# Kernel tuning notes

Hardware: AMD Instinct MI355X
Metric: run time of the kernel (lower is better)

Reference implementation:

```python
import jax, jax.numpy as jnp
import numpy as np

B, T, C, H = 2, 2048, 1024, 16
HD = C // H  # head dim = 64


def setup_inputs() -> dict:
    key = jax.random.key(0)
    k1, k2, k3 = jax.random.split(key, 3)
    scale = 0.02
    x = jax.random.normal(k1, (B, T, C), dtype=jnp.float32)
    w_attn = jax.random.normal(k2, (C, 3 * C), dtype=jnp.float32) * scale
    b_attn = jnp.zeros((3 * C,), dtype=jnp.float32)
    w_proj = jax.random.normal(k3, (C, C), dtype=jnp.float32) * scale
    b_proj = jnp.zeros((C,), dtype=jnp.float32)
    return {"x": x, "w_attn": w_attn, "b_attn": b_attn, "w_proj": w_proj, "b_proj": b_proj}


def reference(x, w_attn, b_attn, w_proj, b_proj):
    b, t, c = x.shape
    qkv = x @ w_attn + b_attn  # [B,T,3C]
    q, k, v = jnp.split(qkv, 3, axis=-1)
    # [B,T,C] -> [B,H,T,HD]
    q = q.reshape(b, t, H, HD).transpose(0, 2, 1, 3)
    k = k.reshape(b, t, H, HD).transpose(0, 2, 1, 3)
    v = v.reshape(b, t, H, HD).transpose(0, 2, 1, 3)
    att = jnp.einsum('bhqd,bhkd->bhqk', q, k) * (1.0 / jnp.sqrt(jnp.float32(HD)))
    causal = jnp.tril(jnp.ones((t, t), dtype=bool))  # [T,T]
    att = jnp.where(causal[None, None, :, :], att, jnp.float32(-jnp.inf))
    att = jax.nn.softmax(att, axis=-1)
    y = jnp.einsum('bhqk,bhkd->bhqd', att, v)
    y = y.transpose(0, 2, 1, 3).reshape(b, t, c)
    return y @ w_proj + b_proj
```

## Files before the change

kernel.cpp:

```cpp
#include <hip/hip_runtime.h>


typedef unsigned short u16;
typedef unsigned short u16x8 __attribute__((ext_vector_type(8)));
typedef __bf16 bf16x8 __attribute__((ext_vector_type(8)));
typedef __bf16 bf16x4 __attribute__((ext_vector_type(4)));
typedef float f32x4 __attribute__((ext_vector_type(4)));

#define MFMA16(a, b, c) __builtin_amdgcn_mfma_f32_16x16x32_bf16(a, b, c, 0, 0, 0)

static __device__ __forceinline__ u16 f2b(float f) {
  union { float f; unsigned int i; } x; x.f = f;
  unsigned int r = x.i + 0x7fffu + ((x.i >> 16) & 1u);
  return (u16)(r >> 16);
}
static __device__ __forceinline__ float b2f(u16 u) {
  union { unsigned int i; float f; } x; x.i = ((unsigned int)u) << 16; return x.f;
}

static __device__ __forceinline__ void gload_lds16(const u16* g, u16* l) {
#if defined(__HIP_DEVICE_COMPILE__)
  __builtin_amdgcn_global_load_lds(
      (const __attribute__((address_space(1))) unsigned int*)g,
      (__attribute__((address_space(3))) unsigned int*)l,
      16, 0, 0);
#else
  (void)g; (void)l;
#endif
}

__global__ __launch_bounds__(256) void cast_f32_bf16(
    const float* __restrict__ in, u16* __restrict__ out) {
  int i = (blockIdx.x * 256 + threadIdx.x) * 8;
  float4 a = *(const float4*)&in[i];
  float4 b = *(const float4*)&in[i + 4];
  u16x8 o;
  o[0] = f2b(a.x); o[1] = f2b(a.y); o[2] = f2b(a.z); o[3] = f2b(a.w);
  o[4] = f2b(b.x); o[5] = f2b(b.y); o[6] = f2b(b.z); o[7] = f2b(b.w);
  *(u16x8*)&out[i] = o;
}

__global__ __launch_bounds__(256) void transpose_f32_bf16(
    const float* __restrict__ in, u16* __restrict__ out, int R, int Cc) {
  __shared__ u16 tile[32][33];
  int bx = blockIdx.x, by = blockIdx.y;
  int tx = threadIdx.x, ty = threadIdx.y;
#pragma unroll
  for (int i = 0; i < 4; i++) {
    int r = by * 32 + ty + i * 8;
    int c = bx * 32 + tx;
    tile[ty + i * 8][tx] = f2b(in[r * Cc + c]);
  }
  __syncthreads();
#pragma unroll
  for (int i = 0; i < 4; i++) {
    int r = bx * 32 + ty + i * 8;
    int c = by * 32 + tx;
    out[r * R + c] = tile[tx][ty + i * 8];
  }
}

__global__ __launch_bounds__(256) void transpose_v(
    const u16* __restrict__ in, u16* __restrict__ out) {
  int bh = blockIdx.y;
  int t = blockIdx.x * 128 + (threadIdx.x & 127);
  int dg = (threadIdx.x >> 7) * 32;
  const u16* src = in + (bh * 2048 + t) * 64;
  u16* dst = out + bh * 64 * 2048 + t;
#pragma unroll
  for (int i = 0; i < 32; i++) {
    int d = dg + i;
    dst[d * 2048] = src[d];
  }
}

template <int MODE>
__global__ __launch_bounds__(256, 2) void gemm_bt(
    const u16* __restrict__ A, const u16* __restrict__ Bt,
    const float* __restrict__ bias, float* __restrict__ out,
    u16* __restrict__ Qb, u16* __restrict__ Kb, u16* __restrict__ Vb,
    int M, int N, int K) {
  __shared__ u16 lA[128 * 32];
  __shared__ u16 lB[128 * 32];

  const int tid = threadIdx.x;
  const int lane = tid & 63;
  const int w = tid >> 6;
  const int wm = (w >> 1) * 64, wn = (w & 1) * 64;
  const int l15 = lane & 15, quad = lane >> 4;
  const int m0 = blockIdx.y * 128, n0 = blockIdx.x * 128;

  const int srow = lane >> 2;
  const int scol = (lane & 3) * 8;

  f32x4 acc[4][4] = {};

  for (int k0 = 0; k0 < K; k0 += 32) {
    __syncthreads();
#pragma unroll
    for (int h = 0; h < 2; h++) {
      int r = h * 64 + w * 16 + srow;
      gload_lds16(&A[(m0 + r) * K + k0 + scol], &lA[h * 2048 + w * 512 + lane * 8]);
      gload_lds16(&Bt[(n0 + r) * K + k0 + scol], &lB[h * 2048 + w * 512 + lane * 8]);
    }
    __syncthreads();

    bf16x8 af[4], bfr[4];
#pragma unroll
    for (int mi = 0; mi < 4; mi++)
      af[mi] = *(const bf16x8*)&lA[(wm + mi * 16 + l15) * 32 + quad * 8];
#pragma unroll
    for (int ni = 0; ni < 4; ni++)
      bfr[ni] = *(const bf16x8*)&lB[(wn + ni * 16 + l15) * 32 + quad * 8];
#pragma unroll
    for (int mi = 0; mi < 4; mi++)
#pragma unroll
      for (int ni = 0; ni < 4; ni++)
        acc[mi][ni] = MFMA16(af[mi], bfr[ni], acc[mi][ni]);
  }

#pragma unroll
  for (int mi = 0; mi < 4; mi++) {
#pragma unroll
    for (int ni = 0; ni < 4; ni++) {
      int n = n0 + wn + ni * 16 + l15;
      float bv = bias[n];
#pragma unroll
      for (int reg = 0; reg < 4; reg++) {
        int m = m0 + wm + mi * 16 + quad * 4 + reg;
        float v = acc[mi][ni][reg] + bv;
        if (MODE == 1) {
          out[m * N + n] = v;
        } else {
          int which = n >> 10;
          if (which == 1) v *= 0.18033688011112042f;
          int hn = n & 1023;
          int hh = hn >> 6, d = hn & 63;
          int b = m >> 11, t = m & 2047;
          u16* dst = (which == 0) ? Qb : ((which == 1) ? Kb : Vb);
          dst[(((b << 4) + hh) * 2048 + t) * 64 + d] = f2b(v);
        }
      }
    }
  }
}

__global__ __launch_bounds__(256, 4) void attn_split(
    const u16* __restrict__ Qg, const u16* __restrict__ Kg,
    const u16* __restrict__ Vt, u16* __restrict__ Yg,
    u16* __restrict__ Opart, float* __restrict__ lpart) {
  __shared__ u16 lk[64 * 72];
  __shared__ u16 lvt[64 * 72];

  const int x = blockIdx.x;
  const int bh = blockIdx.y;
  int qt, s, ns;
  if (x < 8)       { qt = x;                s = 0;            ns = 1; }
  else if (x < 24) { int r = x - 8;  qt = 8  + (r >> 1); s = r & 1; ns = 2; }
  else if (x < 48) { int r = x - 24; qt = 16 + r / 3;    s = r % 3; ns = 3; }
  else             { int r = x - 48; qt = 24 + (r >> 2); s = r & 3; ns = 4; }
  const int kts = s * 8;
  const int kend = (kts + 8 < qt + 1) ? (kts + 8) : (qt + 1);

  const int tid = threadIdx.x;
  const int lane = tid & 63;
  const int w = tid >> 6;
  const int l15 = lane & 15, quad = lane >> 4;
  const int qbase = qt * 64;
  const int base = bh * 2048 * 64;
  const int vbase = bh * 64 * 2048;

  const int sr = tid >> 3;
  const int sc = (tid & 7) * 8;

  const u16* qrow = Qg + base + (qbase + w * 16 + l15) * 64;
  bf16x8 bq0 = *(const bf16x8*)&qrow[quad * 8];
  bf16x8 bq1 = *(const bf16x8*)&qrow[32 + quad * 8];

  u16x8 onesu = {0x3F80, 0x3F80, 0x3F80, 0x3F80, 0x3F80, 0x3F80, 0x3F80, 0x3F80};
  bf16x8 ones = *(const bf16x8*)&onesu;

  const u16* kp = Kg + base;
  const u16* vp = Vt + vbase;

  u16x8 kr[2], vr[2];
  {
    int kvb = kts * 64;
#pragma unroll
    for (int h = 0; h < 2; h++) {
      int r = sr + h * 32;
      kr[h] = *(const u16x8*)&kp[(kvb + r) * 64 + sc];
      vr[h] = *(const u16x8*)&vp[r * 2048 + kvb + sc];
    }
  }

  f32x4 oacc[4] = {};
  f32x4 lacc = {};

  for (int kt = kts; kt < kend; kt++) {
    __syncthreads();
#pragma unroll
    for (int h = 0; h < 2; h++) {
      int r = sr + h * 32;
      *(u16x8*)&lk[r * 72 + sc] = kr[h];
      *(u16x8*)&lvt[r * 72 + sc] = vr[h];
    }
    __syncthreads();
    if (kt + 1 < kend) {
      int kvb = (kt + 1) * 64;
#pragma unroll
      for (int h = 0; h < 2; h++) {
        int r = sr + h * 32;
        kr[h] = *(const u16x8*)&kp[(kvb + r) * 64 + sc];
        vr[h] = *(const u16x8*)&vp[r * 2048 + kvb + sc];
      }
    }

    const bool diag = (kt == qt);
    const int qloc = w * 16 + l15;

#pragma unroll
    for (int u = 0; u < 2; u++) {
      bf16x8 pa;
#pragma unroll
      for (int half = 0; half < 2; half++) {
        int nt = 2 * u + half;
        bf16x8 ak0 = *(const bf16x8*)&lk[(nt * 16 + l15) * 72 + quad * 8];
        bf16x8 ak1 = *(const bf16x8*)&lk[(nt * 16 + l15) * 72 + 32 + quad * 8];
        f32x4 st = {};
        st = MFMA16(ak0, bq0, st);
        st = MFMA16(ak1, bq1, st);
#pragma unroll
        for (int reg = 0; reg < 4; reg++) {
          float sv = st[reg];
          if (diag && (nt * 16 + quad * 4 + reg) > qloc) sv = -1e30f;
          pa[half * 4 + reg] = (__bf16)exp2f(sv);
        }
      }
      lacc = MFMA16(pa, ones, lacc);
#pragma unroll
      for (int dt = 0; dt < 4; dt++) {
        const u16* vrow = &lvt[(dt * 16 + l15) * 72 + u * 32 + quad * 4];
        bf16x4 lo = *(const bf16x4*)&vrow[0];
        bf16x4 hi = *(const bf16x4*)&vrow[16];
        bf16x8 bv;
#pragma unroll
        for (int j = 0; j < 4; j++) { bv[j] = lo[j]; bv[4 + j] = hi[j]; }
        oacc[dt] = MFMA16(pa, bv, oacc[dt]);
      }
    }
  }

  if (ns == 1) {
    const int b = bh >> 4, hh = bh & 15;
    float inv[4];
#pragma unroll
    for (int reg = 0; reg < 4; reg++) inv[reg] = 1.0f / lacc[reg];
#pragma unroll
    for (int dt = 0; dt < 4; dt++)
#pragma unroll
      for (int reg = 0; reg < 4; reg++) {
        int q = qbase + w * 16 + quad * 4 + reg;
        int col = hh * 64 + dt * 16 + l15;
        Yg[(b * 2048 + q) * 1024 + col] = f2b(oacc[dt][reg] * inv[reg]);
      }
  } else {
    const int p = bh * 80 + x;
    u16* op = Opart + p * 4096 + (w * 16) * 64;
#pragma unroll
    for (int dt = 0; dt < 4; dt++)
#pragma unroll
      for (int reg = 0; reg < 4; reg++)
        op[(quad * 4 + reg) * 64 + dt * 16 + l15] = f2b(oacc[dt][reg]);
    if (l15 == 0) {
#pragma unroll
      for (int reg = 0; reg < 4; reg++)
        lpart[p * 64 + w * 16 + quad * 4 + reg] = lacc[reg];
    }
  }
}

__global__ __launch_bounds__(256) void attn_combine(
    const u16* __restrict__ Opart, const float* __restrict__ lpart,
    u16* __restrict__ Yg) {
  const int qt = 8 + blockIdx.x;
  const int bh = blockIdx.y;
  const int tid = threadIdx.x;
  const int row = tid >> 2;
  const int cg = (tid & 3) * 16;
  int xb, ns;
  if (qt < 16)      { xb = 8  + (qt - 8) * 2;  ns = 2; }
  else if (qt < 24) { xb = 24 + (qt - 16) * 3; ns = 3; }
  else              { xb = 48 + (qt - 24) * 4; ns = 4; }

  float acc[16] = {};
  float lsum = 0.f;
  for (int i = 0; i < ns; i++) {
    int p = bh * 80 + xb + i;
    lsum += lpart[p * 64 + row];
    const u16* oprow = Opart + p * 4096 + row * 64 + cg;
    u16x8 a = *(const u16x8*)&oprow[0];
    u16x8 b = *(const u16x8*)&oprow[8];
#pragma unroll
    for (int j = 0; j < 8; j++) { acc[j] += b2f(a[j]); acc[8 + j] += b2f(b[j]); }
  }
  float inv = 1.0f / lsum;
  u16x8 o0, o1;
#pragma unroll
  for (int j = 0; j < 8; j++) { o0[j] = f2b(acc[j] * inv); o1[j] = f2b(acc[8 + j] * inv); }
  const int b = bh >> 4, hh = bh & 15;
  u16* y = Yg + ((long)(b * 2048 + qt * 64 + row)) * 1024 + hh * 64 + cg;
  *(u16x8*)&y[0] = o0;
  *(u16x8*)&y[8] = o1;
}

__global__ __launch_bounds__(256, 4) void attn_kernel(
    const u16* __restrict__ Qg, const u16* __restrict__ Kg,
    const u16* __restrict__ Vt, u16* __restrict__ Yg) {
  __shared__ u16 lk[64 * 72];
  __shared__ u16 lvt[64 * 72];

  const int qt = 31 - blockIdx.x;
  const int bh = blockIdx.y;
  const int tid = threadIdx.x;
  const int lane = tid & 63;
  const int w = tid >> 6;
  const int l15 = lane & 15, quad = lane >> 4;
  const int qbase = qt * 64;
  const int base = bh * 2048 * 64;
  const int vbase = bh * 64 * 2048;
  const int sr = tid >> 3;
  const int sc = (tid & 7) * 8;

  const u16* qrow = Qg + base + (qbase + w * 16 + l15) * 64;
  bf16x8 bq0 = *(const bf16x8*)&qrow[quad * 8];
  bf16x8 bq1 = *(const bf16x8*)&qrow[32 + quad * 8];

  u16x8 onesu = {0x3F80, 0x3F80, 0x3F80, 0x3F80, 0x3F80, 0x3F80, 0x3F80, 0x3F80};
  bf16x8 ones = *(const bf16x8*)&onesu;

  const u16* kp = Kg + base;
  const u16* vp = Vt + vbase;

  u16x8 kr[2], vr[2];
#pragma unroll
  for (int h = 0; h < 2; h++) {
    int r = sr + h * 32;
    kr[h] = *(const u16x8*)&kp[r * 64 + sc];
    vr[h] = *(const u16x8*)&vp[r * 2048 + sc];
  }

  f32x4 oacc[4] = {};
  f32x4 lacc = {};

  for (int kt = 0; kt <= qt; kt++) {
    __syncthreads();
#pragma unroll
    for (int h = 0; h < 2; h++) {
      int r = sr + h * 32;
      *(u16x8*)&lk[r * 72 + sc] = kr[h];
      *(u16x8*)&lvt[r * 72 + sc] = vr[h];
    }
    __syncthreads();
    if (kt < qt) {
      int kvb = (kt + 1) * 64;
#pragma unroll
      for (int h = 0; h < 2; h++) {
        int r = sr + h * 32;
        kr[h] = *(const u16x8*)&kp[(kvb + r) * 64 + sc];
        vr[h] = *(const u16x8*)&vp[r * 2048 + kvb + sc];
      }
    }

    const bool diag = (kt == qt);
    const int qloc = w * 16 + l15;
#pragma unroll
    for (int u = 0; u < 2; u++) {
      bf16x8 pa;
#pragma unroll
      for (int half = 0; half < 2; half++) {
        int nt = 2 * u + half;
        bf16x8 ak0 = *(const bf16x8*)&lk[(nt * 16 + l15) * 72 + quad * 8];
        bf16x8 ak1 = *(const bf16x8*)&lk[(nt * 16 + l15) * 72 + 32 + quad * 8];
        f32x4 st = {};
        st = MFMA16(ak0, bq0, st);
        st = MFMA16(ak1, bq1, st);
#pragma unroll
        for (int reg = 0; reg < 4; reg++) {
          float sv = st[reg];
          if (diag && (nt * 16 + quad * 4 + reg) > qloc) sv = -1e30f;
          pa[half * 4 + reg] = (__bf16)exp2f(sv);
        }
      }
      lacc = MFMA16(pa, ones, lacc);
#pragma unroll
      for (int dt = 0; dt < 4; dt++) {
        const u16* vrow = &lvt[(dt * 16 + l15) * 72 + u * 32 + quad * 4];
        bf16x4 lo = *(const bf16x4*)&vrow[0];
        bf16x4 hi = *(const bf16x4*)&vrow[16];
        bf16x8 bv;
#pragma unroll
        for (int j = 0; j < 4; j++) { bv[j] = lo[j]; bv[4 + j] = hi[j]; }
        oacc[dt] = MFMA16(pa, bv, oacc[dt]);
      }
    }
  }

  const int b = bh >> 4, hh = bh & 15;
  float inv[4];
#pragma unroll
  for (int reg = 0; reg < 4; reg++) inv[reg] = 1.0f / lacc[reg];
#pragma unroll
  for (int dt = 0; dt < 4; dt++)
#pragma unroll
    for (int reg = 0; reg < 4; reg++) {
      int q = qbase + w * 16 + quad * 4 + reg;
      int col = hh * 64 + dt * 16 + l15;
      Yg[(b * 2048 + q) * 1024 + col] = f2b(oacc[dt][reg] * inv[reg]);
    }
}

extern "C" void kernel_launch(void* const* d_in, const int* in_sizes, int n_in,
                              void* d_out, int out_size, void* d_ws, size_t ws_size,
                              hipStream_t stream) {
  const float* x      = (const float*)d_in[0];
  const float* w_attn = (const float*)d_in[1];
  const float* b_attn = (const float*)d_in[2];
  const float* w_proj = (const float*)d_in[3];
  const float* b_proj = (const float*)d_in[4];
  float* out = (float*)d_out;

  char* ws = (char*)d_ws;
  u16* wattnT = (u16*)(ws);
  u16* wprojT = (u16*)(ws + 6291456);
  u16* xb     = (u16*)(ws + 8388608);
  u16* Vt     = xb;
  u16* Qb     = (u16*)(ws + 16777216);
  u16* Kb     = (u16*)(ws + 25165824);
  u16* Vb     = (u16*)(ws + 33554432);
  u16* Yb     = (u16*)(ws + 41943040);
  u16* Opart  = (u16*)(ws + 50331648);
  float* lpart = (float*)(ws + 71303168);

  const bool split = (ws_size >= 71958528ULL);

  cast_f32_bf16<<<2048, 256, 0, stream>>>(x, xb);
  transpose_f32_bf16<<<dim3(96, 32), dim3(32, 8), 0, stream>>>(w_attn, wattnT, 1024, 3072);
  transpose_f32_bf16<<<dim3(32, 32), dim3(32, 8), 0, stream>>>(w_proj, wprojT, 1024, 1024);
  gemm_bt<0><<<dim3(24, 32), 256, 0, stream>>>(xb, wattnT, b_attn, nullptr,
                                               Qb, Kb, Vb, 4096, 3072, 1024);
  transpose_v<<<dim3(16, 32), 256, 0, stream>>>(Vb, Vt);
  if (split) {
    attn_split<<<dim3(80, 32), 256, 0, stream>>>(Qb, Kb, Vt, Yb, Opart, lpart);
    attn_combine<<<dim3(24, 32), 256, 0, stream>>>(Opart, lpart, Yb);
  } else {
    attn_kernel<<<dim3(32, 32), 256, 0, stream>>>(Qb, Kb, Vt, Yb);
  }
  gemm_bt<1><<<dim3(8, 32), 256, 0, stream>>>(Yb, wprojT, b_proj, out,
                                              nullptr, nullptr, nullptr, 4096, 1024, 1024);
}
```

Before: 198.2 us.

## Permute V-transpose layout, double-buffer attention LDS, balance key splits

The V transpose now writes tokens in a permuted order within each 32-token group. This lets the attention kernels read each V fragment as a single 8-wide LDS load instead of two 4-wide loads plus a shuffle. The split-attention kernel double-buffers its K/V shared tiles, removing one barrier per iteration. It also divides key tiles evenly across splits rather than in fixed chunks of 8. Smaller changes swap exp2f for the hardware exp2 builtin and raise the GEMM occupancy hint to 3 blocks, which may add register pressure or spills.

```diff
diff --git a/kernel.cpp b/kernel.cpp
--- a/kernel.cpp
+++ b/kernel.cpp
@@ -66,7 +66,9 @@
   int t = blockIdx.x * 128 + (threadIdx.x & 127);
   int dg = (threadIdx.x >> 7) * 32;
   const u16* src = in + (bh * 2048 + t) * 64;
-  u16* dst = out + bh * 64 * 2048 + t;
+  int p = t & 31;
+  int tp = (t & ~31) | ((((p >> 2) & 3) << 3) | ((p >> 4) << 2) | (p & 3));
+  u16* dst = out + bh * 64 * 2048 + tp;
 #pragma unroll
   for (int i = 0; i < 32; i++) {
     int d = dg + i;
@@ -75,7 +77,7 @@
 }
 
 template <int MODE>
-__global__ __launch_bounds__(256, 2) void gemm_bt(
+__global__ __launch_bounds__(256, 3) void gemm_bt(
     const u16* __restrict__ A, const u16* __restrict__ Bt,
     const float* __restrict__ bias, float* __restrict__ out,
     u16* __restrict__ Qb, u16* __restrict__ Kb, u16* __restrict__ Vb,
@@ -149,8 +151,8 @@
     const u16* __restrict__ Qg, const u16* __restrict__ Kg,
     const u16* __restrict__ Vt, u16* __restrict__ Yg,
     u16* __restrict__ Opart, float* __restrict__ lpart) {
-  __shared__ u16 lk[64 * 72];
-  __shared__ u16 lvt[64 * 72];
+  __shared__ u16 lk[2][64 * 72];
+  __shared__ u16 lvt[2][64 * 72];
 
   const int x = blockIdx.x;
   const int bh = blockIdx.y;
@@ -159,8 +161,9 @@
   else if (x < 24) { int r = x - 8;  qt = 8  + (r >> 1); s = r & 1; ns = 2; }
   else if (x < 48) { int r = x - 24; qt = 16 + r / 3;    s = r % 3; ns = 3; }
   else             { int r = x - 48; qt = 24 + (r >> 2); s = r & 3; ns = 4; }
-  const int kts = s * 8;
-  const int kend = (kts + 8 < qt + 1) ? (kts + 8) : (qt + 1);
+  const int total = qt + 1;
+  const int kts  = (s * total) / ns;
+  const int kend = ((s + 1) * total) / ns;
 
   const int tid = threadIdx.x;
   const int lane = tid & 63;
@@ -169,6 +172,7 @@
   const int qbase = qt * 64;
   const int base = bh * 2048 * 64;
   const int vbase = bh * 64 * 2048;
+  const int qloc = w * 16 + l15;
 
   const int sr = tid >> 3;
   const int sc = (tid & 7) * 8;
@@ -197,13 +201,15 @@
   f32x4 oacc[4] = {};
   f32x4 lacc = {};
 
+  int cur = 0;
   for (int kt = kts; kt < kend; kt++) {
-    __syncthreads();
+    u16* lkc = lk[cur];
+    u16* lvc = lvt[cur];
 #pragma unroll
     for (int h = 0; h < 2; h++) {
       int r = sr + h * 32;
-      *(u16x8*)&lk[r * 72 + sc] = kr[h];
-      *(u16x8*)&lvt[r * 72 + sc] = vr[h];
+      *(u16x8*)&lkc[r * 72 + sc] = kr[h];
+      *(u16x8*)&lvc[r * 72 + sc] = vr[h];
     }
     __syncthreads();
     if (kt + 1 < kend) {
@@ -217,7 +223,6 @@
     }
 
     const bool diag = (kt == qt);
-    const int qloc = w * 16 + l15;
 
 #pragma unroll
     for (int u = 0; u < 2; u++) {
@@ -225,8 +230,8 @@
 #pragma unroll
       for (int half = 0; half < 2; half++) {
         int nt = 2 * u + half;
-        bf16x8 ak0 = *(const bf16x8*)&lk[(nt * 16 + l15) * 72 + quad * 8];
-        bf16x8 ak1 = *(const bf16x8*)&lk[(nt * 16 + l15) * 72 + 32 + quad * 8];
+        bf16x8 ak0 = *(const bf16x8*)&lkc[(nt * 16 + l15) * 72 + quad * 8];
+        bf16x8 ak1 = *(const bf16x8*)&lkc[(nt * 16 + l15) * 72 + 32 + quad * 8];
         f32x4 st = {};
         st = MFMA16(ak0, bq0, st);
         st = MFMA16(ak1, bq1, st);
@@ -234,21 +239,17 @@
         for (int reg = 0; reg < 4; reg++) {
           float sv = st[reg];
           if (diag && (nt * 16 + quad * 4 + reg) > qloc) sv = -1e30f;
-          pa[half * 4 + reg] = (__bf16)exp2f(sv);
+          pa[half * 4 + reg] = (__bf16)__builtin_amdgcn_exp2f(sv);
         }
       }
       lacc = MFMA16(pa, ones, lacc);
 #pragma unroll
       for (int dt = 0; dt < 4; dt++) {
-        const u16* vrow = &lvt[(dt * 16 + l15) * 72 + u * 32 + quad * 4];
-        bf16x4 lo = *(const bf16x4*)&vrow[0];
-        bf16x4 hi = *(const bf16x4*)&vrow[16];
-        bf16x8 bv;
-#pragma unroll
-        for (int j = 0; j < 4; j++) { bv[j] = lo[j]; bv[4 + j] = hi[j]; }
+        bf16x8 bv = *(const bf16x8*)&lvc[(dt * 16 + l15) * 72 + u * 32 + quad * 8];
         oacc[dt] = MFMA16(pa, bv, oacc[dt]);
       }
     }
+    cur ^= 1;
   }
 
   if (ns == 1) {
@@ -389,18 +390,13 @@
         for (int reg = 0; reg < 4; reg++) {
           float sv = st[reg];
           if (diag && (nt * 16 + quad * 4 + reg) > qloc) sv = -1e30f;
-          pa[half * 4 + reg] = (__bf16)exp2f(sv);
+          pa[half * 4 + reg] = (__bf16)__builtin_amdgcn_exp2f(sv);
         }
       }
       lacc = MFMA16(pa, ones, lacc);
 #pragma unroll
       for (int dt = 0; dt < 4; dt++) {
-        const u16* vrow = &lvt[(dt * 16 + l15) * 72 + u * 32 + quad * 4];
-        bf16x4 lo = *(const bf16x4*)&vrow[0];
-        bf16x4 hi = *(const bf16x4*)&vrow[16];
-        bf16x8 bv;
-#pragma unroll
-        for (int j = 0; j < 4; j++) { bv[j] = lo[j]; bv[4 + j] = hi[j]; }
+        bf16x8 bv = *(const bf16x8*)&lvt[(dt * 16 + l15) * 72 + u * 32 + quad * 8];
         oacc[dt] = MFMA16(pa, bv, oacc[dt]);
       }
     }
```

After: 195.1 us. Within noise of the previous version (-1.5%).
